# Performance work log

Hardware: AMD Instinct MI355X
Metric: run time of the kernel (lower is better)

## Reference

```python
import jax, jax.numpy as jnp
import numpy as np

N_INST = 8  # max instance id; ids 1..N_INST, 0 = background
MESH_NORM = 1024.0  # from SegmantationLoss._meshgrid


def _meshgrid(H, W):
    y = jnp.arange(H, dtype=jnp.float32) / MESH_NORM
    x = jnp.arange(W, dtype=jnp.float32) / MESH_NORM
    return jnp.stack([jnp.broadcast_to(y[:, None], (H, W)),
                      jnp.broadcast_to(x[None, :], (H, W))], axis=0)  # [2,H,W]


def _lovasz_hinge_batch(logits, labels, delta=1.0):
    """logits, labels: [K,P] float. Returns [K] lovasz hinge losses."""
    signs = 2.0 * labels - 1.0
    errors = delta - logits * signs
    order = jnp.argsort(-errors, axis=1)  # descending
    es = jnp.take_along_axis(errors, order, axis=1)
    gs = jnp.take_along_axis(labels, order, axis=1)
    gts = gs.sum(axis=1, keepdims=True)
    intersection = gts - jnp.cumsum(gs, axis=1)
    union = gts + jnp.cumsum(1.0 - gs, axis=1)
    jac = 1.0 - intersection / union
    grad = jnp.concatenate([jac[:, :1], jac[:, 1:] - jac[:, :-1]], axis=1)
    return (jax.nn.relu(es) * grad).sum(axis=1)


def setup_inputs() -> dict:
    key = jax.random.key(0)
    k1, k2, k3, k4 = jax.random.split(key, 4)
    B, H, W = 4, 512, 1024
    x_vec = jax.random.normal(k1, (B, 2, H, W), dtype=jnp.float32)
    # small scale so psigma = exp(10*ppsigma) stays in a sane range
    x_sigma = jax.random.normal(k2, (B, 2, H, W), dtype=jnp.float32) * 0.03
    x_seed = jax.random.normal(k3, (B, 1, H, W), dtype=jnp.float32)
    t = jax.random.randint(k4, (B, H, W), 0, 9, dtype=jnp.int32)
    return {"x_vec": x_vec, "x_sigma": x_sigma, "x_seed": x_seed, "t": t}


def reference(x_vec, x_sigma, x_seed, t):
    B, _, H, W = x_vec.shape
    mesh = _meshgrid(H, W)

    emb = jnp.tanh(x_vec) + mesh[None]          # [B,2,H,W] spatial embedding
    ppsig = x_sigma                              # [B,2,H,W] pre-pseudo-sigma
    seed = jax.nn.sigmoid(x_seed)[:, 0]          # [B,H,W]

    ids = jnp.arange(1, N_INST + 1, dtype=t.dtype)
    mf = (t[None] == ids[:, None, None, None]).astype(jnp.float32)  # [N,B,H,W]
    cnt = mf.sum(axis=(2, 3))                    # [N,B]
    present = cnt > 0
    safe = jnp.maximum(cnt, 1.0)
    n_present = jnp.maximum(present.sum(axis=0).astype(jnp.float32), 1.0)  # [B]

    # per-instance masked means
    centroid = jnp.einsum('nbhw,bchw->nbc', mf, emb) / safe[..., None]    # [N,B,2]
    inst_pps = jnp.einsum('nbhw,bchw->nbc', mf, ppsig) / safe[..., None]  # [N,B,2]
    psigma = jnp.exp(10.0 * inst_pps)                                     # [N,B,2]

    # gaussian between pixel and instance embedding (l22n)
    diff2 = (emb[None] - centroid[..., None, None]) ** 2                  # [N,B,2,H,W]
    dist = (diff2 * psigma[..., None, None]).sum(axis=2)                  # [N,B,H,W]
    gauss = jnp.exp(-0.5 * dist)                                          # [N,B,H,W]

    # lovasz hinge per instance on logits 2*gauss - 1 over all pixels
    P = H * W
    lov = _lovasz_hinge_batch((2.0 * gauss - 1.0).reshape(N_INST * B, P),
                              mf.reshape(N_INST * B, P)).reshape(N_INST, B)
    lov = jnp.where(present, lov, 0.0)
    lovasz_loss = (lov.sum(axis=0) / n_present).mean()

    # sigma loss: pixel ppsigma -> detached instance mean ppsigma
    sd = (ppsig[None] - jax.lax.stop_gradient(inst_pps)[..., None, None]) ** 2
    sl = (sd.sum(axis=2) * mf).sum(axis=(2, 3)) / safe                    # [N,B]
    sl = jnp.where(present, sl, 0.0)
    sigma_loss = (sl.sum(axis=0) / n_present).mean()

    # seed loss: background -> 0, foreground -> detached gaussian
    bg = (t == 0).astype(jnp.float32)                                     # [B,H,W]
    bg_cnt = jnp.maximum(bg.sum(axis=(1, 2)), 1.0)
    bg_loss = ((seed ** 2) * bg).sum(axis=(1, 2)) / bg_cnt                # [B]
    fg = ((seed[None] - jax.lax.stop_gradient(gauss)) ** 2 * mf).sum(axis=(2, 3)) / safe
    fg = jnp.where(present, fg, 0.0)
    seed_loss = ((bg_loss + fg.sum(axis=0)) /
                 (1.0 + present.sum(axis=0).astype(jnp.float32))).mean()

    return lovasz_loss + sigma_loss + seed_loss
```

## Files before the change

kernel.cpp:

```cpp
#include <hip/hip_runtime.h>
#include <math.h>

#define B 4
#define H 512
#define W 1024
#define P (H*W)
#define NI 8
#define NSEG 32
#define NB 1024
#define INV_BW ((float)NB/2.0f)
#define NSTRIP 128
#define STRIP_PX (P/NSTRIP)
#define K1B 512
#define K1PX (P/K1B)

#define D_CENY 0
#define D_CENX 32
#define D_PSY  64
#define D_PSX  96
#define D_CNT  128
#define D_SL   160
#define D_BGL  192
#define OFF_FGP 256
#define OFF_HIST (256 + NI*512)
#define OFF_PK1  OFF_HIST

__device__ __forceinline__ float fast_tanh(float x) {
    float e = __expf(2.0f * x);
    return 1.0f - 2.0f / (e + 1.0f);
}
__device__ __forceinline__ float fast_sigmoid(float x) {
    return 1.0f / (1.0f + __expf(-x));
}

template<int CTRL, int RM>
__device__ __forceinline__ float dpp_add(float x) {
    int y = __builtin_amdgcn_update_dpp(0, __float_as_int(x), CTRL, RM, 0xF, true);
    return x + __int_as_float(y);
}
__device__ __forceinline__ float wred(float x) {
    x = dpp_add<0x111, 0xF>(x);
    x = dpp_add<0x112, 0xF>(x);
    x = dpp_add<0x114, 0xF>(x);
    x = dpp_add<0x118, 0xF>(x);
    x = dpp_add<0x142, 0xA>(x);
    x = dpp_add<0x143, 0xC>(x);
    return x;
}

__global__ __launch_bounds__(256) void k1_stats(const float* __restrict__ xv,
                                                const float* __restrict__ xs,
                                                const float* __restrict__ xseed,
                                                const int*  __restrict__ t,
                                                float* __restrict__ pk1) {
    const int b = blockIdx.y, bx = blockIdx.x, tid = threadIdx.x;
    const int lane = tid & 63, wid = tid >> 6;
    const float* xv_y = xv + (size_t)b*2*P;
    const float* xv_x = xv_y + P;
    const float* xs_y = xs + (size_t)b*2*P;
    const float* xs_x = xs_y + P;
    const float* sdp  = xseed + (size_t)b*P;
    const int*   tb   = t + (size_t)b*P;

    float cnt[NI], sey[NI], sex[NI], sgy[NI], sgx[NI], sq[NI];
    #pragma unroll
    for (int n = 0; n < NI; ++n) { cnt[n]=0.f; sey[n]=0.f; sex[n]=0.f; sgy[n]=0.f; sgx[n]=0.f; sq[n]=0.f; }
    float bgc = 0.f, bgs = 0.f;

    int p0 = bx*K1PX + tid*4;
    float4 vy = *(const float4*)(xv_y + p0);
    float4 vx = *(const float4*)(xv_x + p0);
    float4 sy = *(const float4*)(xs_y + p0);
    float4 sx = *(const float4*)(xs_x + p0);
    float4 se = *(const float4*)(sdp + p0);
    int4   tt = *(const int4*)(tb + p0);
    #pragma unroll
    for (int j = 0; j < 4; ++j) {
        int pix = p0 + j;
        float ey = fast_tanh((&vy.x)[j]) + (float)(pix >> 10) * (1.0f/1024.0f);
        float ex = fast_tanh((&vx.x)[j]) + (float)(pix & 1023) * (1.0f/1024.0f);
        float gy = (&sy.x)[j], gx = (&sx.x)[j];
        int tv = (&tt.x)[j];
        if (tv == 0) {
            float s = fast_sigmoid((&se.x)[j]);
            bgc += 1.f; bgs += s*s;
        }
        float q = gy*gy + gx*gx;
        #pragma unroll
        for (int n = 0; n < NI; ++n) {
            float m = (tv == n+1) ? 1.0f : 0.0f;
            cnt[n] += m; sey[n] += m*ey; sex[n] += m*ex;
            sgy[n] += m*gy; sgx[n] += m*gx; sq[n] += m*q;
        }
    }
    __shared__ float sw[4*64];
    #define RED50(val, slot) { float r_ = wred(val); if (lane == 63) sw[wid*64 + (slot)] = r_; }
    #pragma unroll
    for (int n = 0; n < NI; ++n) {
        RED50(cnt[n], n*6+0); RED50(sey[n], n*6+1); RED50(sex[n], n*6+2);
        RED50(sgy[n], n*6+3); RED50(sgx[n], n*6+4); RED50(sq[n],  n*6+5);
    }
    RED50(bgc, 48); RED50(bgs, 49);
    #undef RED50
    __syncthreads();
    if (tid < 50) {
        float s = sw[tid] + sw[64+tid] + sw[128+tid] + sw[192+tid];
        pk1[(size_t)(b*K1B + bx)*64 + tid] = s;
    }
}

__global__ __launch_bounds__(1024) void k2_finalize(float* __restrict__ wsf,
                                                    const float* __restrict__ pk1,
                                                    float* __restrict__ out) {
    const int tid = threadIdx.x;
    __shared__ float part[16*64];
    __shared__ float ssum[4*64];
    const int v = tid & 63, g = tid >> 6;
    const int b = g >> 2, c = g & 3;
    float acc = 0.f;
    const int jbase = b*K1B + c*128;
    #pragma unroll 8
    for (int i = 0; i < 128; ++i) acc += pk1[(size_t)(jbase + i)*64 + v];
    part[g*64 + v] = acc;
    __syncthreads();
    if (tid < 256) {
        int vb = tid & 63, bb = tid >> 6;
        ssum[bb*64+vb] = part[(bb*4+0)*64+vb] + part[(bb*4+1)*64+vb]
                       + part[(bb*4+2)*64+vb] + part[(bb*4+3)*64+vb];
    }
    __syncthreads();
    if (tid < NSEG) {
        int n = tid >> 2, bb = tid & 3;
        float cv  = ssum[bb*64 + n*6+0];
        float sey = ssum[bb*64 + n*6+1];
        float sex = ssum[bb*64 + n*6+2];
        float sgy = ssum[bb*64 + n*6+3];
        float sgx = ssum[bb*64 + n*6+4];
        float sq  = ssum[bb*64 + n*6+5];
        float safe = fmaxf(cv, 1.0f);
        float ipy = sgy/safe, ipx = sgx/safe;
        wsf[D_CENY+tid] = sey/safe;
        wsf[D_CENX+tid] = sex/safe;
        wsf[D_PSY+tid]  = expf(10.0f*ipy);
        wsf[D_PSX+tid]  = expf(10.0f*ipx);
        wsf[D_CNT+tid]  = cv;
        wsf[D_SL+tid]   = sq/safe - (ipy*ipy + ipx*ipx);
    } else if (tid < NSEG + B) {
        int bb = tid - NSEG;
        wsf[D_BGL+bb] = ssum[bb*64+49] / fmaxf(ssum[bb*64+48], 1.0f);
    } else if (tid == 40) {
        out[0] = 0.f;
    }
}

__global__ __launch_bounds__(512) void k3_hist(const float* __restrict__ xv,
                                               const float* __restrict__ xseed,
                                               const int*  __restrict__ t,
                                               const float* __restrict__ wsf,
                                               unsigned* __restrict__ hist_g,
                                               float* __restrict__ fgp) {
    const int strip = blockIdx.x;
    const int b     = blockIdx.y;
    const int tid   = threadIdx.x;
    const int lane  = tid & 63;

    __shared__ unsigned hist[NI*NB];
    for (int i = tid; i < NI*NB; i += 512) hist[i] = 0u;
    __shared__ float spar[4*NI];
    if (tid < 4*NI) {
        int n = tid & (NI-1), q = tid >> 3;
        spar[tid] = wsf[q*32 + n*B + b];
    }
    __syncthreads();

    float ceny[NI], cenx[NI], psy[NI], psx[NI], fgn[NI];
    #pragma unroll
    for (int n = 0; n < NI; ++n) {
        ceny[n] = spar[n]; cenx[n] = spar[NI+n];
        psy[n] = spar[2*NI+n]; psx[n] = spar[3*NI+n];
        fgn[n] = 0.f;
    }

    const float* xv_y = xv + (size_t)b*2*P;
    const float* xv_x = xv_y + P;
    const float* sdp  = xseed + (size_t)b*P;
    const int*   tb   = t + (size_t)b*P;
    const int base = strip * STRIP_PX;

    #pragma unroll
    for (int it = 0; it < STRIP_PX/2048; ++it) {
        int p0 = base + it*2048 + tid*4;
        float4 vy = *(const float4*)(xv_y + p0);
        float4 vx = *(const float4*)(xv_x + p0);
        float4 se = *(const float4*)(sdp + p0);
        int4   tt = *(const int4*)(tb + p0);
        #pragma unroll
        for (int j = 0; j < 4; ++j) {
            int pix = p0 + j;
            float ey = fast_tanh((&vy.x)[j]) + (float)(pix >> 10) * (1.0f/1024.0f);
            float ex = fast_tanh((&vx.x)[j]) + (float)(pix & 1023) * (1.0f/1024.0f);
            int tv = (&tt.x)[j];
            float gown = 0.f;
            #pragma unroll
            for (int n = 0; n < NI; ++n) {
                float dy = ey - ceny[n], dx = ex - cenx[n];
                float g = __expf(-0.5f * (psy[n]*dy*dy + psx[n]*dx*dx));
                bool lab = (tv == n+1);
                float err = lab ? (2.0f - 2.0f*g) : (2.0f*g);
                int key = (int)(err * INV_BW);
                key = key > (NB-1) ? (NB-1) : key;
                if (key > 0) atomicAdd(&hist[n*NB + key], lab ? 0x10000u : 1u);
                if (lab) gown = g;
            }
            if (tv > 0) {
                float s = fast_sigmoid((&se.x)[j]);
                float d = s - gown;
                float dd = d*d;
                #pragma unroll
                for (int n = 0; n < NI; ++n) fgn[n] += (tv == n+1) ? dd : 0.f;
            }
        }
    }
    __syncthreads();
    for (int i = tid; i < NI*NB; i += 512) {
        int n = i >> 10, key = i & (NB-1);
        int seg = n*B + b;
        hist_g[((size_t)(seg*NSTRIP + strip))*NB + key] = hist[i];
    }
    __shared__ float sfg[NI];
    if (tid < NI) sfg[tid] = 0.f;
    __syncthreads();
    #pragma unroll
    for (int n = 0; n < NI; ++n) {
        float r = wred(fgn[n]);
        if (lane == 63 && r != 0.f) atomicAdd(&sfg[n], r);
    }
    __syncthreads();
    if (tid < NI) fgp[tid*512 + b*NSTRIP + strip] = sfg[tid];
}

__global__ __launch_bounds__(256) void k4_final(const unsigned* __restrict__ hist_g,
                                                const float* __restrict__ wsf,
                                                const float* __restrict__ fgp,
                                                float* __restrict__ out) {
    const int seg = blockIdx.x, tid = threadIdx.x;
    const int n = seg >> 2, b = seg & 3;
    __shared__ float scnt[NSEG];
    if (tid < NSEG) scnt[tid] = wsf[D_CNT + tid];
    __syncthreads();

    if (seg == 0 && tid == 0) {
        float add = 0.f;
        for (int bb = 0; bb < B; ++bb) {
            int np = 0; float ss = 0.f;
            for (int k = 0; k < NI; ++k) {
                float c = scnt[k*4 + bb];
                if (c > 0.5f) { np++; ss += wsf[D_SL + k*4 + bb]; }
            }
            float npf = fmaxf((float)np, 1.0f);
            add += ss/npf + wsf[D_BGL+bb] / (1.0f + (float)np);
        }
        atomicAdd(out, add * (1.0f/(float)B));
    }

    const float G = scnt[seg];
    if (G < 0.5f) return;
    int npc = 0;
    #pragma unroll
    for (int k = 0; k < NI; ++k) npc += (scnt[k*4 + b] > 0.5f) ? 1 : 0;

    __shared__ float sfr[128];
    if (tid < 128) sfr[tid] = fgp[n*512 + b*NSTRIP + tid];
    __syncthreads();
    #pragma unroll
    for (int d = 64; d > 0; d >>= 1) {
        if (tid < d) sfr[tid] += sfr[tid + d];
        __syncthreads();
    }
    const float FG = sfr[0];

    unsigned pos4[4] = {0u,0u,0u,0u}, neg4[4] = {0u,0u,0u,0u};
    const uint4* hp = (const uint4*)(hist_g + (size_t)seg*NSTRIP*NB) + tid;
    #pragma unroll 8
    for (int s = 0; s < NSTRIP; ++s) {
        uint4 v = hp[(size_t)s*(NB/4)];
        pos4[0] += v.x >> 16; neg4[0] += v.x & 0xffffu;
        pos4[1] += v.y >> 16; neg4[1] += v.y & 0xffffu;
        pos4[2] += v.z >> 16; neg4[2] += v.z & 0xffffu;
        pos4[3] += v.w >> 16; neg4[3] += v.w & 0xffffu;
    }
    unsigned tp = pos4[0]+pos4[1]+pos4[2]+pos4[3];
    unsigned tn = neg4[0]+neg4[1]+neg4[2]+neg4[3];

    __shared__ unsigned up[256], un[256];
    up[tid] = tp; un[tid] = tn;
    __syncthreads();
    for (int d = 1; d < 256; d <<= 1) {
        unsigned ap = (tid + d < 256) ? up[tid + d] : 0u;
        unsigned an = (tid + d < 256) ? un[tid + d] : 0u;
        __syncthreads();
        up[tid] += ap; un[tid] += an;
        __syncthreads();
    }
    const unsigned TP = up[0], TN = un[0];
    const unsigned Gu = (unsigned)(G + 0.5f);
    const unsigned NEGu = (unsigned)P - Gu;
    unsigned cump = up[tid] - tp;
    unsigned cumn = un[tid] - tn;

    const double dG = (double)G;
    double acc = 0.0;
    #pragma unroll
    for (int j = 3; j >= 0; --j) {
        unsigned cp = pos4[j], cn = neg4[j];
        int key = tid*4 + j;
        if (tid == 0 && j == 0) { cp = Gu - TP; cn = NEGu - TN; }
        if (cp | cn) {
            unsigned ep = cump, en = cumn;
            unsigned epi = ep + cp, eni = en + cn;
            double jb = 1.0 - (dG - (double)ep)  / (dG + (double)en);
            double ja = 1.0 - (dG - (double)epi) / (dG + (double)eni);
            acc += (((double)key + 0.5) * (2.0/(double)NB)) * (ja - jb);
        }
        cump += cp; cumn += cn;
    }
    __shared__ double sdd[256];
    sdd[tid] = acc;
    __syncthreads();
    #pragma unroll
    for (int d = 128; d > 0; d >>= 1) {
        if (tid < d) sdd[tid] += sdd[tid + d];
        __syncthreads();
    }
    if (tid == 0) {
        float npf = fmaxf((float)npc, 1.0f);
        float val = (float)sdd[0] / (npf * (float)B)
                  + (FG / G) / ((1.0f + (float)npc) * (float)B);
        atomicAdd(out, val);
    }
}

extern "C" void kernel_launch(void* const* d_in, const int* in_sizes, int n_in,
                              void* d_out, int out_size, void* d_ws, size_t ws_size,
                              hipStream_t stream) {
    (void)in_sizes; (void)n_in; (void)out_size; (void)ws_size;
    const float* xv  = (const float*)d_in[0];
    const float* xs  = (const float*)d_in[1];
    const float* xsd = (const float*)d_in[2];
    const int*   t   = (const int*)d_in[3];
    float* wsf = (float*)d_ws;
    unsigned* hist_g = (unsigned*)d_ws + OFF_HIST;
    float* pk1 = wsf + OFF_PK1;
    float* fgp = wsf + OFF_FGP;
    float* out = (float*)d_out;

    k1_stats<<<dim3(K1B, B), 256, 0, stream>>>(xv, xs, xsd, t, pk1);
    k2_finalize<<<1, 1024, 0, stream>>>(wsf, pk1, out);
    k3_hist<<<dim3(NSTRIP, B), 512, 0, stream>>>(xv, xsd, t, wsf, hist_g, fgp);
    k4_final<<<NSEG, 256, 0, stream>>>(hist_g, wsf, fgp, out);
}
```

Baseline: 139.6 us.

## Fuse four kernels into one cooperative kernel with register-cached pixel data

Replaces the four-kernel pipeline with a single cooperative kernel that uses grid syncs between phases. Each block keeps its embeddings, sigmoid values and packed labels in registers, so the histogram phase does not re-read inputs or recompute tanh and sigmoid. Histogram partials are folded in parallel across all blocks before a final per-segment scan. The costs are higher register pressure, the overhead of four grid-wide syncs, and only 256 resident blocks doing all the work.

Result: slower. 240.1 us (+71.9%).

```diff
diff --git a/kernel.cpp b/kernel.cpp
--- a/kernel.cpp
+++ b/kernel.cpp
@@ -1,18 +1,19 @@
 #include <hip/hip_runtime.h>
+#include <hip/hip_cooperative_groups.h>
 #include <math.h>
 
+namespace cg = cooperative_groups;
+
 #define B 4
-#define H 512
-#define W 1024
-#define P (H*W)
+#define P (512*1024)
 #define NI 8
 #define NSEG 32
 #define NB 1024
-#define INV_BW ((float)NB/2.0f)
-#define NSTRIP 128
-#define STRIP_PX (P/NSTRIP)
-#define K1B 512
-#define K1PX (P/K1B)
+#define INV_BW 512.0f
+#define NCHUNK 64
+#define CHUNK_PX 8192
+#define NBLK 256
+#define NTHR 512
 
 #define D_CENY 0
 #define D_CENX 32
@@ -21,9 +22,10 @@
 #define D_CNT  128
 #define D_SL   160
 #define D_BGL  192
-#define OFF_FGP 256
-#define OFF_HIST (256 + NI*512)
-#define OFF_PK1  OFF_HIST
+#define OFF_PK1  256
+#define OFF_FGP  (OFF_PK1 + NBLK*64)
+#define OFF_FOLD (OFF_FGP + NSEG*NCHUNK)
+#define OFF_HIST (OFF_FOLD + 2*NSEG*NB)
 
 __device__ __forceinline__ float fast_tanh(float x) {
     float e = __expf(2.0f * x);
@@ -32,7 +34,6 @@
 __device__ __forceinline__ float fast_sigmoid(float x) {
     return 1.0f / (1.0f + __expf(-x));
 }
-
 template<int CTRL, int RM>
 __device__ __forceinline__ float dpp_add(float x) {
     int y = __builtin_amdgcn_update_dpp(0, __float_as_int(x), CTRL, RM, 0xF, true);
@@ -48,295 +49,303 @@
     return x;
 }
 
-__global__ __launch_bounds__(256) void k1_stats(const float* __restrict__ xv,
-                                                const float* __restrict__ xs,
-                                                const float* __restrict__ xseed,
-                                                const int*  __restrict__ t,
-                                                float* __restrict__ pk1) {
-    const int b = blockIdx.y, bx = blockIdx.x, tid = threadIdx.x;
+__global__ __launch_bounds__(NTHR, 2) void fused_all(const float* __restrict__ xv,
+                                                     const float* __restrict__ xs,
+                                                     const float* __restrict__ xseed,
+                                                     const int*  __restrict__ t,
+                                                     float* __restrict__ wsf,
+                                                     unsigned* __restrict__ hist_g,
+                                                     float* __restrict__ out) {
+    cg::grid_group grid = cg::this_grid();
+    const int bid = blockIdx.x;
+    const int c   = bid >> 2;
+    const int b   = bid & 3;
+    const int tid = threadIdx.x;
     const int lane = tid & 63, wid = tid >> 6;
-    const float* xv_y = xv + (size_t)b*2*P;
-    const float* xv_x = xv_y + P;
-    const float* xs_y = xs + (size_t)b*2*P;
-    const float* xs_x = xs_y + P;
-    const float* sdp  = xseed + (size_t)b*P;
-    const int*   tb   = t + (size_t)b*P;
-
-    float cnt[NI], sey[NI], sex[NI], sgy[NI], sgx[NI], sq[NI];
-    #pragma unroll
-    for (int n = 0; n < NI; ++n) { cnt[n]=0.f; sey[n]=0.f; sex[n]=0.f; sgy[n]=0.f; sgx[n]=0.f; sq[n]=0.f; }
-    float bgc = 0.f, bgs = 0.f;
-
-    int p0 = bx*K1PX + tid*4;
-    float4 vy = *(const float4*)(xv_y + p0);
-    float4 vx = *(const float4*)(xv_x + p0);
-    float4 sy = *(const float4*)(xs_y + p0);
-    float4 sx = *(const float4*)(xs_x + p0);
-    float4 se = *(const float4*)(sdp + p0);
-    int4   tt = *(const int4*)(tb + p0);
-    #pragma unroll
-    for (int j = 0; j < 4; ++j) {
-        int pix = p0 + j;
-        float ey = fast_tanh((&vy.x)[j]) + (float)(pix >> 10) * (1.0f/1024.0f);
-        float ex = fast_tanh((&vx.x)[j]) + (float)(pix & 1023) * (1.0f/1024.0f);
-        float gy = (&sy.x)[j], gx = (&sx.x)[j];
-        int tv = (&tt.x)[j];
-        if (tv == 0) {
-            float s = fast_sigmoid((&se.x)[j]);
-            bgc += 1.f; bgs += s*s;
-        }
-        float q = gy*gy + gx*gx;
+
+    __shared__ unsigned shm[NI*NB];
+    __shared__ float sw[8*64];
+    __shared__ float sfg8[NI];
+    __shared__ float scnt32[NSEG];
+
+    float* pk1 = wsf + OFF_PK1;
+    float* fgp = wsf + OFF_FGP;
+    unsigned* fold = (unsigned*)wsf + OFF_FOLD;
+
+    float eys[16], exs[16], ssg[16];
+    unsigned tvp[2] = {0u, 0u};
+
+    {
+        const float* xv_y = xv + (size_t)b*2*P;
+        const float* xv_x = xv_y + P;
+        const float* xs_y = xs + (size_t)b*2*P;
+        const float* xs_x = xs_y + P;
+        const float* sdp  = xseed + (size_t)b*P;
+        const int*   tb   = t + (size_t)b*P;
+        const int base = c * CHUNK_PX;
+
+        float cnt[NI], sey[NI], sex[NI], sgy[NI], sgx[NI], sq[NI];
+        #pragma unroll
+        for (int n = 0; n < NI; ++n) { cnt[n]=0.f; sey[n]=0.f; sex[n]=0.f; sgy[n]=0.f; sgx[n]=0.f; sq[n]=0.f; }
+        float bgc = 0.f, bgs = 0.f;
+
+        #pragma unroll
+        for (int it = 0; it < 4; ++it) {
+            int p0 = base + it*2048 + tid*4;
+            float4 vy = *(const float4*)(xv_y + p0);
+            float4 vx = *(const float4*)(xv_x + p0);
+            float4 sy = *(const float4*)(xs_y + p0);
+            float4 sx = *(const float4*)(xs_x + p0);
+            float4 se = *(const float4*)(sdp + p0);
+            int4   tt = *(const int4*)(tb + p0);
+            #pragma unroll
+            for (int j = 0; j < 4; ++j) {
+                int idx = it*4 + j;
+                int pix = p0 + j;
+                float ey = fast_tanh((&vy.x)[j]) + (float)(pix >> 10) * (1.0f/1024.0f);
+                float ex = fast_tanh((&vx.x)[j]) + (float)(pix & 1023) * (1.0f/1024.0f);
+                float gy = (&sy.x)[j], gx = (&sx.x)[j];
+                float s  = fast_sigmoid((&se.x)[j]);
+                int tv = (&tt.x)[j];
+                eys[idx] = ey; exs[idx] = ex; ssg[idx] = s;
+                tvp[idx >> 3] |= ((unsigned)tv) << ((idx & 7)*4);
+                if (tv == 0) { bgc += 1.f; bgs += s*s; }
+                float q = gy*gy + gx*gx;
+                #pragma unroll
+                for (int n = 0; n < NI; ++n) {
+                    float m = (tv == n+1) ? 1.0f : 0.0f;
+                    cnt[n] += m; sey[n] += m*ey; sex[n] += m*ex;
+                    sgy[n] += m*gy; sgx[n] += m*gx; sq[n] += m*q;
+                }
+            }
+        }
+        #define RED50(val, slot) { float r_ = wred(val); if (lane == 63) sw[wid*64 + (slot)] = r_; }
         #pragma unroll
         for (int n = 0; n < NI; ++n) {
-            float m = (tv == n+1) ? 1.0f : 0.0f;
-            cnt[n] += m; sey[n] += m*ey; sex[n] += m*ex;
-            sgy[n] += m*gy; sgx[n] += m*gx; sq[n] += m*q;
-        }
-    }
-    __shared__ float sw[4*64];
-    #define RED50(val, slot) { float r_ = wred(val); if (lane == 63) sw[wid*64 + (slot)] = r_; }
-    #pragma unroll
-    for (int n = 0; n < NI; ++n) {
-        RED50(cnt[n], n*6+0); RED50(sey[n], n*6+1); RED50(sex[n], n*6+2);
-        RED50(sgy[n], n*6+3); RED50(sgx[n], n*6+4); RED50(sq[n],  n*6+5);
-    }
-    RED50(bgc, 48); RED50(bgs, 49);
-    #undef RED50
-    __syncthreads();
-    if (tid < 50) {
-        float s = sw[tid] + sw[64+tid] + sw[128+tid] + sw[192+tid];
-        pk1[(size_t)(b*K1B + bx)*64 + tid] = s;
-    }
-}
-
-__global__ __launch_bounds__(1024) void k2_finalize(float* __restrict__ wsf,
-                                                    const float* __restrict__ pk1,
-                                                    float* __restrict__ out) {
-    const int tid = threadIdx.x;
-    __shared__ float part[16*64];
-    __shared__ float ssum[4*64];
-    const int v = tid & 63, g = tid >> 6;
-    const int b = g >> 2, c = g & 3;
-    float acc = 0.f;
-    const int jbase = b*K1B + c*128;
-    #pragma unroll 8
-    for (int i = 0; i < 128; ++i) acc += pk1[(size_t)(jbase + i)*64 + v];
-    part[g*64 + v] = acc;
-    __syncthreads();
-    if (tid < 256) {
-        int vb = tid & 63, bb = tid >> 6;
-        ssum[bb*64+vb] = part[(bb*4+0)*64+vb] + part[(bb*4+1)*64+vb]
-                       + part[(bb*4+2)*64+vb] + part[(bb*4+3)*64+vb];
-    }
-    __syncthreads();
-    if (tid < NSEG) {
-        int n = tid >> 2, bb = tid & 3;
-        float cv  = ssum[bb*64 + n*6+0];
-        float sey = ssum[bb*64 + n*6+1];
-        float sex = ssum[bb*64 + n*6+2];
-        float sgy = ssum[bb*64 + n*6+3];
-        float sgx = ssum[bb*64 + n*6+4];
-        float sq  = ssum[bb*64 + n*6+5];
-        float safe = fmaxf(cv, 1.0f);
-        float ipy = sgy/safe, ipx = sgx/safe;
-        wsf[D_CENY+tid] = sey/safe;
-        wsf[D_CENX+tid] = sex/safe;
-        wsf[D_PSY+tid]  = expf(10.0f*ipy);
-        wsf[D_PSX+tid]  = expf(10.0f*ipx);
-        wsf[D_CNT+tid]  = cv;
-        wsf[D_SL+tid]   = sq/safe - (ipy*ipy + ipx*ipx);
-    } else if (tid < NSEG + B) {
-        int bb = tid - NSEG;
-        wsf[D_BGL+bb] = ssum[bb*64+49] / fmaxf(ssum[bb*64+48], 1.0f);
-    } else if (tid == 40) {
-        out[0] = 0.f;
-    }
-}
-
-__global__ __launch_bounds__(512) void k3_hist(const float* __restrict__ xv,
-                                               const float* __restrict__ xseed,
-                                               const int*  __restrict__ t,
-                                               const float* __restrict__ wsf,
-                                               unsigned* __restrict__ hist_g,
-                                               float* __restrict__ fgp) {
-    const int strip = blockIdx.x;
-    const int b     = blockIdx.y;
-    const int tid   = threadIdx.x;
-    const int lane  = tid & 63;
-
-    __shared__ unsigned hist[NI*NB];
-    for (int i = tid; i < NI*NB; i += 512) hist[i] = 0u;
-    __shared__ float spar[4*NI];
-    if (tid < 4*NI) {
-        int n = tid & (NI-1), q = tid >> 3;
-        spar[tid] = wsf[q*32 + n*B + b];
-    }
-    __syncthreads();
-
-    float ceny[NI], cenx[NI], psy[NI], psx[NI], fgn[NI];
-    #pragma unroll
-    for (int n = 0; n < NI; ++n) {
-        ceny[n] = spar[n]; cenx[n] = spar[NI+n];
-        psy[n] = spar[2*NI+n]; psx[n] = spar[3*NI+n];
-        fgn[n] = 0.f;
-    }
-
-    const float* xv_y = xv + (size_t)b*2*P;
-    const float* xv_x = xv_y + P;
-    const float* sdp  = xseed + (size_t)b*P;
-    const int*   tb   = t + (size_t)b*P;
-    const int base = strip * STRIP_PX;
-
-    #pragma unroll
-    for (int it = 0; it < STRIP_PX/2048; ++it) {
-        int p0 = base + it*2048 + tid*4;
-        float4 vy = *(const float4*)(xv_y + p0);
-        float4 vx = *(const float4*)(xv_x + p0);
-        float4 se = *(const float4*)(sdp + p0);
-        int4   tt = *(const int4*)(tb + p0);
-        #pragma unroll
-        for (int j = 0; j < 4; ++j) {
-            int pix = p0 + j;
-            float ey = fast_tanh((&vy.x)[j]) + (float)(pix >> 10) * (1.0f/1024.0f);
-            float ex = fast_tanh((&vx.x)[j]) + (float)(pix & 1023) * (1.0f/1024.0f);
-            int tv = (&tt.x)[j];
-            float gown = 0.f;
-            #pragma unroll
-            for (int n = 0; n < NI; ++n) {
-                float dy = ey - ceny[n], dx = ex - cenx[n];
-                float g = __expf(-0.5f * (psy[n]*dy*dy + psx[n]*dx*dx));
-                bool lab = (tv == n+1);
-                float err = lab ? (2.0f - 2.0f*g) : (2.0f*g);
-                int key = (int)(err * INV_BW);
-                key = key > (NB-1) ? (NB-1) : key;
-                if (key > 0) atomicAdd(&hist[n*NB + key], lab ? 0x10000u : 1u);
-                if (lab) gown = g;
-            }
-            if (tv > 0) {
-                float s = fast_sigmoid((&se.x)[j]);
-                float d = s - gown;
-                float dd = d*d;
+            RED50(cnt[n], n*6+0); RED50(sey[n], n*6+1); RED50(sex[n], n*6+2);
+            RED50(sgy[n], n*6+3); RED50(sgx[n], n*6+4); RED50(sq[n],  n*6+5);
+        }
+        RED50(bgc, 48); RED50(bgs, 49);
+        #undef RED50
+        __syncthreads();
+        if (tid < 50) {
+            float s = 0.f;
+            #pragma unroll
+            for (int w = 0; w < 8; ++w) s += sw[w*64 + tid];
+            pk1[(size_t)bid*64 + tid] = s;
+        }
+    }
+    grid.sync();
+
+    if (bid == 0) {
+        float* part = (float*)shm;
+        const int v = tid & 63, g = tid >> 6;
+        const int bb = g & 3, h = g >> 2;
+        float acc = 0.f;
+        #pragma unroll 8
+        for (int i = 0; i < 32; ++i) {
+            int cc = h*32 + i;
+            acc += pk1[(size_t)(cc*4 + bb)*64 + v];
+        }
+        part[g*64 + v] = acc;
+        __syncthreads();
+        if (tid < 256) {
+            int b2 = tid >> 6, v2 = tid & 63;
+            part[b2*64 + v2] = part[b2*64 + v2] + part[(b2+4)*64 + v2];
+        }
+        __syncthreads();
+        if (tid < NSEG) {
+            int n = tid >> 2, b2 = tid & 3;
+            float cv  = part[b2*64 + n*6+0];
+            float sey = part[b2*64 + n*6+1];
+            float sex = part[b2*64 + n*6+2];
+            float sgy = part[b2*64 + n*6+3];
+            float sgx = part[b2*64 + n*6+4];
+            float sq  = part[b2*64 + n*6+5];
+            float safe = fmaxf(cv, 1.0f);
+            float ipy = sgy/safe, ipx = sgx/safe;
+            wsf[D_CENY+tid] = sey/safe;
+            wsf[D_CENX+tid] = sex/safe;
+            wsf[D_PSY+tid]  = expf(10.0f*ipy);
+            wsf[D_PSX+tid]  = expf(10.0f*ipx);
+            wsf[D_CNT+tid]  = cv;
+            wsf[D_SL+tid]   = sq/safe - (ipy*ipy + ipx*ipx);
+        } else if (tid < NSEG + B) {
+            int b2 = tid - NSEG;
+            wsf[D_BGL+b2] = part[b2*64+49] / fmaxf(part[b2*64+48], 1.0f);
+        } else if (tid == 40) {
+            out[0] = 0.f;
+        }
+    }
+    grid.sync();
+
+    {
+        for (int i = tid; i < NI*NB; i += NTHR) shm[i] = 0u;
+        float ceny[NI], cenx[NI], psy[NI], psx[NI], fgn[NI];
+        #pragma unroll
+        for (int n = 0; n < NI; ++n) {
+            ceny[n] = wsf[D_CENY + n*4 + b];
+            cenx[n] = wsf[D_CENX + n*4 + b];
+            psy[n]  = wsf[D_PSY  + n*4 + b];
+            psx[n]  = wsf[D_PSX  + n*4 + b];
+            fgn[n]  = 0.f;
+        }
+        if (tid < NI) sfg8[tid] = 0.f;
+        __syncthreads();
+
+        #pragma unroll
+        for (int it = 0; it < 4; ++it) {
+            #pragma unroll
+            for (int j = 0; j < 4; ++j) {
+                int idx = it*4 + j;
+                float ey = eys[idx], ex = exs[idx];
+                int tv = (int)((tvp[idx >> 3] >> ((idx & 7)*4)) & 0xFu);
+                float gown = 0.f;
                 #pragma unroll
-                for (int n = 0; n < NI; ++n) fgn[n] += (tv == n+1) ? dd : 0.f;
-            }
-        }
-    }
-    __syncthreads();
-    for (int i = tid; i < NI*NB; i += 512) {
-        int n = i >> 10, key = i & (NB-1);
-        int seg = n*B + b;
-        hist_g[((size_t)(seg*NSTRIP + strip))*NB + key] = hist[i];
-    }
-    __shared__ float sfg[NI];
-    if (tid < NI) sfg[tid] = 0.f;
-    __syncthreads();
-    #pragma unroll
-    for (int n = 0; n < NI; ++n) {
-        float r = wred(fgn[n]);
-        if (lane == 63 && r != 0.f) atomicAdd(&sfg[n], r);
-    }
-    __syncthreads();
-    if (tid < NI) fgp[tid*512 + b*NSTRIP + strip] = sfg[tid];
-}
-
-__global__ __launch_bounds__(256) void k4_final(const unsigned* __restrict__ hist_g,
-                                                const float* __restrict__ wsf,
-                                                const float* __restrict__ fgp,
-                                                float* __restrict__ out) {
-    const int seg = blockIdx.x, tid = threadIdx.x;
-    const int n = seg >> 2, b = seg & 3;
-    __shared__ float scnt[NSEG];
-    if (tid < NSEG) scnt[tid] = wsf[D_CNT + tid];
-    __syncthreads();
-
-    if (seg == 0 && tid == 0) {
-        float add = 0.f;
-        for (int bb = 0; bb < B; ++bb) {
-            int np = 0; float ss = 0.f;
-            for (int k = 0; k < NI; ++k) {
-                float c = scnt[k*4 + bb];
-                if (c > 0.5f) { np++; ss += wsf[D_SL + k*4 + bb]; }
-            }
-            float npf = fmaxf((float)np, 1.0f);
-            add += ss/npf + wsf[D_BGL+bb] / (1.0f + (float)np);
-        }
-        atomicAdd(out, add * (1.0f/(float)B));
-    }
-
-    const float G = scnt[seg];
-    if (G < 0.5f) return;
-    int npc = 0;
-    #pragma unroll
-    for (int k = 0; k < NI; ++k) npc += (scnt[k*4 + b] > 0.5f) ? 1 : 0;
-
-    __shared__ float sfr[128];
-    if (tid < 128) sfr[tid] = fgp[n*512 + b*NSTRIP + tid];
-    __syncthreads();
-    #pragma unroll
-    for (int d = 64; d > 0; d >>= 1) {
-        if (tid < d) sfr[tid] += sfr[tid + d];
-        __syncthreads();
-    }
-    const float FG = sfr[0];
-
-    unsigned pos4[4] = {0u,0u,0u,0u}, neg4[4] = {0u,0u,0u,0u};
-    const uint4* hp = (const uint4*)(hist_g + (size_t)seg*NSTRIP*NB) + tid;
-    #pragma unroll 8
-    for (int s = 0; s < NSTRIP; ++s) {
-        uint4 v = hp[(size_t)s*(NB/4)];
-        pos4[0] += v.x >> 16; neg4[0] += v.x & 0xffffu;
-        pos4[1] += v.y >> 16; neg4[1] += v.y & 0xffffu;
-        pos4[2] += v.z >> 16; neg4[2] += v.z & 0xffffu;
-        pos4[3] += v.w >> 16; neg4[3] += v.w & 0xffffu;
-    }
-    unsigned tp = pos4[0]+pos4[1]+pos4[2]+pos4[3];
-    unsigned tn = neg4[0]+neg4[1]+neg4[2]+neg4[3];
-
-    __shared__ unsigned up[256], un[256];
-    up[tid] = tp; un[tid] = tn;
-    __syncthreads();
-    for (int d = 1; d < 256; d <<= 1) {
-        unsigned ap = (tid + d < 256) ? up[tid + d] : 0u;
-        unsigned an = (tid + d < 256) ? un[tid + d] : 0u;
-        __syncthreads();
-        up[tid] += ap; un[tid] += an;
-        __syncthreads();
-    }
-    const unsigned TP = up[0], TN = un[0];
-    const unsigned Gu = (unsigned)(G + 0.5f);
-    const unsigned NEGu = (unsigned)P - Gu;
-    unsigned cump = up[tid] - tp;
-    unsigned cumn = un[tid] - tn;
-
-    const double dG = (double)G;
-    double acc = 0.0;
-    #pragma unroll
-    for (int j = 3; j >= 0; --j) {
-        unsigned cp = pos4[j], cn = neg4[j];
-        int key = tid*4 + j;
-        if (tid == 0 && j == 0) { cp = Gu - TP; cn = NEGu - TN; }
-        if (cp | cn) {
-            unsigned ep = cump, en = cumn;
-            unsigned epi = ep + cp, eni = en + cn;
-            double jb = 1.0 - (dG - (double)ep)  / (dG + (double)en);
-            double ja = 1.0 - (dG - (double)epi) / (dG + (double)eni);
-            acc += (((double)key + 0.5) * (2.0/(double)NB)) * (ja - jb);
-        }
-        cump += cp; cumn += cn;
-    }
-    __shared__ double sdd[256];
-    sdd[tid] = acc;
-    __syncthreads();
-    #pragma unroll
-    for (int d = 128; d > 0; d >>= 1) {
-        if (tid < d) sdd[tid] += sdd[tid + d];
-        __syncthreads();
-    }
-    if (tid == 0) {
-        float npf = fmaxf((float)npc, 1.0f);
-        float val = (float)sdd[0] / (npf * (float)B)
-                  + (FG / G) / ((1.0f + (float)npc) * (float)B);
-        atomicAdd(out, val);
+                for (int n = 0; n < NI; ++n) {
+                    float dy = ey - ceny[n], dx = ex - cenx[n];
+                    float g = __expf(-0.5f * (psy[n]*dy*dy + psx[n]*dx*dx));
+                    bool lab = (tv == n+1);
+                    float err = lab ? (2.0f - 2.0f*g) : (2.0f*g);
+                    int key = (int)(err * INV_BW);
+                    key = key > (NB-1) ? (NB-1) : key;
+                    if (key > 0) atomicAdd(&shm[n*NB + key], lab ? 0x10000u : 1u);
+                    if (lab) gown = g;
+                }
+                if (tv > 0) {
+                    float d = ssg[idx] - gown;
+                    float dd = d*d;
+                    #pragma unroll
+                    for (int n = 0; n < NI; ++n) fgn[n] += (tv == n+1) ? dd : 0.f;
+                }
+            }
+        }
+        __syncthreads();
+        for (int i = tid; i < NI*NB; i += NTHR) {
+            int n = i >> 10, key = i & (NB-1);
+            hist_g[((size_t)((n*4 + b)*NCHUNK + c))*NB + key] = shm[i];
+        }
+        #pragma unroll
+        for (int n = 0; n < NI; ++n) {
+            float r = wred(fgn[n]);
+            if (lane == 63 && r != 0.f) atomicAdd(&sfg8[n], r);
+        }
+        __syncthreads();
+        if (tid < NI) fgp[(tid*4 + b)*NCHUNK + c] = sfg8[tid];
+    }
+    grid.sync();
+
+    {
+        const int seg = bid >> 3, kb = bid & 7;
+        const int k = tid & 127, sh = tid >> 7;
+        const unsigned* src = hist_g + (size_t)(seg*NCHUNK)*NB + kb*128 + k;
+        unsigned pos = 0u, neg = 0u;
+        #pragma unroll 8
+        for (int cc = sh*16; cc < sh*16 + 16; ++cc) {
+            unsigned v = src[(size_t)cc*NB];
+            pos += v >> 16; neg += v & 0xffffu;
+        }
+        if (tid < 256) shm[tid] = 0u;
+        __syncthreads();
+        atomicAdd(&shm[k], pos);
+        atomicAdd(&shm[128 + k], neg);
+        __syncthreads();
+        if (tid < 128)      fold[(size_t)seg*NB + kb*128 + tid] = shm[tid];
+        else if (tid < 256) fold[(size_t)(NSEG + seg)*NB + kb*128 + (tid-128)] = shm[tid];
+    }
+    grid.sync();
+
+    if (bid < NSEG) {
+        const int seg = bid;
+        const int bb = seg & 3;
+        if (tid < NSEG) scnt32[tid] = wsf[D_CNT + tid];
+        __syncthreads();
+
+        if (seg == 0 && tid == 0) {
+            float add = 0.f;
+            for (int b2 = 0; b2 < B; ++b2) {
+                int np = 0; float ss = 0.f;
+                for (int k = 0; k < NI; ++k) {
+                    float cv = scnt32[k*4 + b2];
+                    if (cv > 0.5f) { np++; ss += wsf[D_SL + k*4 + b2]; }
+                }
+                float npf = fmaxf((float)np, 1.0f);
+                add += ss/npf + wsf[D_BGL+b2] / (1.0f + (float)np);
+            }
+            atomicAdd(out, add * (1.0f/(float)B));
+        }
+
+        const float G = scnt32[seg];
+        if (G >= 0.5f) {
+            int npc = 0;
+            #pragma unroll
+            for (int k = 0; k < NI; ++k) npc += (scnt32[k*4 + bb] > 0.5f) ? 1 : 0;
+
+            float* sfr = (float*)(shm + 3072);
+            if (tid < NCHUNK) sfr[tid] = fgp[seg*NCHUNK + tid];
+            __syncthreads();
+            #pragma unroll
+            for (int d = 32; d > 0; d >>= 1) {
+                if (tid < d) sfr[tid] += sfr[tid + d];
+                __syncthreads();
+            }
+            const float FG = sfr[0];
+
+            uint2 pv = *((const uint2*)(fold + (size_t)seg*NB) + tid);
+            uint2 nv = *((const uint2*)(fold + (size_t)(NSEG + seg)*NB) + tid);
+            unsigned pos2[2] = {pv.x, pv.y};
+            unsigned neg2[2] = {nv.x, nv.y};
+            unsigned tp = pos2[0] + pos2[1];
+            unsigned tn = neg2[0] + neg2[1];
+
+            unsigned* up = shm;
+            unsigned* un = shm + 512;
+            double* sdd = (double*)(shm + 1024);
+            up[tid] = tp; un[tid] = tn;
+            __syncthreads();
+            for (int d = 1; d < NTHR; d <<= 1) {
+                unsigned ap = (tid + d < NTHR) ? up[tid + d] : 0u;
+                unsigned an = (tid + d < NTHR) ? un[tid + d] : 0u;
+                __syncthreads();
+                up[tid] += ap; un[tid] += an;
+                __syncthreads();
+            }
+            const unsigned TP = up[0], TN = un[0];
+            const unsigned Gu = (unsigned)(G + 0.5f);
+            const unsigned NEGu = (unsigned)P - Gu;
+            unsigned cump = up[tid] - tp;
+            unsigned cumn = un[tid] - tn;
+
+            const double dG = (double)G;
+            double acc = 0.0;
+            #pragma unroll
+            for (int j = 1; j >= 0; --j) {
+                unsigned cp = pos2[j], cn = neg2[j];
+                int key = tid*2 + j;
+                if (tid == 0 && j == 0) { cp = Gu - TP; cn = NEGu - TN; }
+                if (cp | cn) {
+                    unsigned ep = cump, en = cumn;
+                    unsigned epi = ep + cp, eni = en + cn;
+                    double jb = 1.0 - (dG - (double)ep)  / (dG + (double)en);
+                    double ja = 1.0 - (dG - (double)epi) / (dG + (double)eni);
+                    acc += (((double)key + 0.5) * (2.0/(double)NB)) * (ja - jb);
+                }
+                cump += cp; cumn += cn;
+            }
+            sdd[tid] = acc;
+            __syncthreads();
+            #pragma unroll
+            for (int d = 256; d > 0; d >>= 1) {
+                if (tid < d) sdd[tid] += sdd[tid + d];
+                __syncthreads();
+            }
+            if (tid == 0) {
+                float npf = fmaxf((float)npc, 1.0f);
+                float val = (float)sdd[0] / (npf * (float)B)
+                          + (FG / G) / ((1.0f + (float)npc) * (float)B);
+                atomicAdd(out, val);
+            }
+        }
     }
 }
 
@@ -350,12 +359,10 @@
     const int*   t   = (const int*)d_in[3];
     float* wsf = (float*)d_ws;
     unsigned* hist_g = (unsigned*)d_ws + OFF_HIST;
-    float* pk1 = wsf + OFF_PK1;
-    float* fgp = wsf + OFF_FGP;
     float* out = (float*)d_out;
 
-    k1_stats<<<dim3(K1B, B), 256, 0, stream>>>(xv, xs, xsd, t, pk1);
-    k2_finalize<<<1, 1024, 0, stream>>>(wsf, pk1, out);
-    k3_hist<<<dim3(NSTRIP, B), 512, 0, stream>>>(xv, xsd, t, wsf, hist_g, fgp);
-    k4_final<<<NSEG, 256, 0, stream>>>(hist_g, wsf, fgp, out);
-}
+    void* args[] = { (void*)&xv, (void*)&xs, (void*)&xsd, (void*)&t,
+                     (void*)&wsf, (void*)&hist_g, (void*)&out };
+    hipLaunchCooperativeKernel((const void*)fused_all, dim3(NBLK), dim3(NTHR),
+                               args, 0, stream);
+}
```
